# Kernel tuning notes

Hardware: AMD Instinct MI355X
Metric: run time of the kernel (lower is better)

Reference implementation:

```python
import jax, jax.numpy as jnp
import numpy as np
from jax import lax

B, C, H, W = 8, 512, 16, 16
Di, N, R, K = 1024, 16, 32, 4  # d_inner, d_state, dt_rank, num scan directions
EPS = 1e-5


def _ln(x, g, b):
    mu = x.mean(-1, keepdims=True)
    var = ((x - mu) ** 2).mean(-1, keepdims=True)
    return (x - mu) * lax.rsqrt(var + EPS) * g + b


def _ss2d_core(xc, x_proj_w, dt_w, dt_b, A_logs, Ds):
    # xc: (b, Di, H, W) after depthwise conv + SiLU. 4-direction selective scan.
    b = xc.shape[0]
    L = H * W
    x_flat = xc.reshape(b, Di, L)
    x_wh = xc.transpose(0, 1, 3, 2).reshape(b, Di, L)
    x_hwwh = jnp.stack([x_flat, x_wh], 1)                  # (b,2,Di,L)
    xs = jnp.concatenate([x_hwwh, x_hwwh[..., ::-1]], 1)   # (b,K,Di,L)
    x_dbl = jnp.einsum('bkdl,kcd->bkcl', xs, x_proj_w)     # (b,K,R+2N,L)
    dts, Bs, Cs = x_dbl[:, :, :R], x_dbl[:, :, R:R + N], x_dbl[:, :, R + N:]
    dts = jnp.einsum('bkrl,kdr->bkdl', dts, dt_w)
    delta = jax.nn.softplus(dts + dt_b[None, :, :, None])  # (b,K,Di,L)
    A = -jnp.exp(A_logs).reshape(K, Di, N)                 # (K,Di,N)

    def step(h, inp):
        d, u, Bl, Cl = inp  # d,u:(b,K,Di)  Bl,Cl:(b,K,N)
        h = jnp.exp(d[..., None] * A) * h + (d * u)[..., None] * Bl[:, :, None, :]
        yl = jnp.einsum('bkdn,bkn->bkd', h, Cl)
        return h, yl

    inps = (delta.transpose(3, 0, 1, 2), xs.transpose(3, 0, 1, 2),
            Bs.transpose(3, 0, 1, 2), Cs.transpose(3, 0, 1, 2))
    h0 = jnp.zeros((b, K, Di, N), xc.dtype)
    _, ys = lax.scan(step, h0, inps)                       # (L,b,K,Di)
    ys = ys.transpose(1, 2, 3, 0) + xs * Ds.reshape(1, K, Di, 1)  # + D*u skip
    inv = ys[:, 2:4, :, ::-1]
    wh = ys[:, 1].reshape(b, Di, W, H).transpose(0, 1, 3, 2).reshape(b, Di, L)
    invwh = inv[:, 1].reshape(b, Di, W, H).transpose(0, 1, 3, 2).reshape(b, Di, L)
    y = ys[:, 0] + inv[:, 0] + wh + invwh                  # (b,Di,L)
    return y.transpose(0, 2, 1).reshape(b, H, W, Di)


def _conv_ffn(x, ffn_conv_w, bn_g, bn_b, bn_mean, bn_var, fc1_w, fc2_w):
    x = lax.conv_general_dilated(x, ffn_conv_w, (1, 1), [(1, 1), (1, 1)],
                                 dimension_numbers=('NCHW', 'OIHW', 'NCHW'))
    x = ((x - bn_mean[:, None, None]) * lax.rsqrt(bn_var + EPS)[:, None, None]
         * bn_g[:, None, None] + bn_b[:, None, None])
    x = jnp.clip(x, 0.0, 6.0)                              # ReLU6
    x = jnp.einsum('bchw,oc->bohw', x, fc1_w)              # 1x1 conv fc1
    x = jax.nn.gelu(x, approximate=False)
    return jnp.einsum('bchw,oc->bohw', x, fc2_w)           # 1x1 conv fc2


def _forward(x, y, ln1_g, ln1_b, in_proj_w, conv_w, conv_b, x_proj_w, dt_w,
             dt_b, A_logs, Ds, out_norm_g, out_norm_b, out_proj_w, ffn_conv_w,
             bn_g, bn_b, bn_mean, bn_var, fc1_w, fc2_w, lin1_w, lin1_b,
             lin2_w, lin2_b):
    # --- VSSBlock: LN -> SS2D -> residual ---
    x1 = x.transpose(0, 2, 3, 1)                           # (B,H,W,C)
    xn = _ln(x1, ln1_g, ln1_b)
    xz = jnp.einsum('bhwc,oc->bhwo', xn, in_proj_w)        # in_proj (no bias)
    xa, z = xz[..., :Di], xz[..., Di:]
    xc = xa.transpose(0, 3, 1, 2)                          # (B,Di,H,W)
    xc = lax.conv_general_dilated(xc, conv_w, (1, 1), [(1, 1), (1, 1)],
                                  feature_group_count=Di,
                                  dimension_numbers=('NCHW', 'OIHW', 'NCHW'))
    xc = jax.nn.silu(xc + conv_b[:, None, None])
    yc = _ss2d_core(xc, x_proj_w, dt_w, dt_b, A_logs, Ds)  # (B,H,W,Di)
    yc = _ln(yc, out_norm_g, out_norm_b) * jax.nn.silu(z)
    vss = x1 + jnp.einsum('bhwd,od->bhwo', yc, out_proj_w)
    # --- ConvFFN ---
    xm = _conv_ffn(vss.transpose(0, 3, 1, 2), ffn_conv_w, bn_g, bn_b, bn_mean,
                   bn_var, fc1_w, fc2_w)                   # (B,C,H,W)
    # --- channel attention: both pools are AdaptiveAvgPool2d(1), so max==avg ---
    pooled = y.mean(axis=(2, 3))                           # (B,C)
    lin = jax.nn.relu(pooled @ lin1_w.T + lin1_b) @ lin2_w.T + lin2_b
    gate = jax.nn.sigmoid(2.0 * lin)                       # linear_max + linear_avg
    return gate[:, :, None, None] * xm


def setup_inputs() -> dict:
    key = jax.random.key(0)
    ks = jax.random.split(key, 16)
    n = lambda i, shape, s=0.05: jax.random.normal(ks[i], shape, jnp.float32) * s
    return {
        'x': n(0, (B, C, H, W), 1.0),
        'y': n(1, (B, C, H, W), 1.0),
        'ln1_g': jnp.ones((C,), jnp.float32), 'ln1_b': jnp.zeros((C,), jnp.float32),
        'in_proj_w': n(2, (2 * Di, C)),
        'conv_w': n(3, (Di, 1, 3, 3), 0.2), 'conv_b': jnp.zeros((Di,), jnp.float32),
        'x_proj_w': n(4, (K, R + 2 * N, Di)),
        'dt_w': n(5, (K, Di, R), 0.1), 'dt_b': n(6, (K, Di), 0.1),
        'A_logs': n(7, (K * Di, N), 0.1), 'Ds': jnp.ones((K * Di,), jnp.float32),
        'out_norm_g': jnp.ones((Di,), jnp.float32), 'out_norm_b': jnp.zeros((Di,), jnp.float32),
        'out_proj_w': n(8, (C, Di)),
        'ffn_conv_w': n(9, (C, C, 3, 3)),
        'bn_g': jnp.ones((C,), jnp.float32), 'bn_b': jnp.zeros((C,), jnp.float32),
        'bn_mean': jnp.zeros((C,), jnp.float32), 'bn_var': jnp.ones((C,), jnp.float32),
        'fc1_w': n(10, (C, C)), 'fc2_w': n(11, (C, C)),
        'lin1_w': n(12, (C // 2, C)), 'lin1_b': jnp.zeros((C // 2,), jnp.float32),
        'lin2_w': n(13, (C, C // 2)), 'lin2_b': jnp.zeros((C,), jnp.float32),
    }


def reference(x, y, ln1_g, ln1_b, in_proj_w, conv_w, conv_b, x_proj_w, dt_w,
              dt_b, A_logs, Ds, out_norm_g, out_norm_b, out_proj_w, ffn_conv_w,
              bn_g, bn_b, bn_mean, bn_var, fc1_w, fc2_w, lin1_w, lin1_b,
              lin2_w, lin2_b):
    return _forward(x, y, ln1_g, ln1_b, in_proj_w, conv_w, conv_b, x_proj_w,
                    dt_w, dt_b, A_logs, Ds, out_norm_g, out_norm_b, out_proj_w,
                    ffn_conv_w, bn_g, bn_b, bn_mean, bn_var, fc1_w, fc2_w,
                    lin1_w, lin1_b, lin2_w, lin2_b)
```

## Files before the change

kernel.cpp:

```cpp
#include <hip/hip_runtime.h>
#include <hip/hip_bf16.h>
#include <math.h>

#define DEV_INLINE __device__ __forceinline__

constexpr int B_ = 8, C_ = 512, L_ = 256;
constexpr float EPS_ = 1e-5f;

typedef __attribute__((ext_vector_type(8))) short bf16x8;
typedef __attribute__((ext_vector_type(4))) float f32x4;

DEV_INLINE int lmap1(int l) { return ((l & 15) << 4) | (l >> 4); }
DEV_INLINE float sigmoidf_(float x) { return 1.f / (1.f + __expf(-x)); }
DEV_INLINE float siluf_(float x) { return x * sigmoidf_(x); }

DEV_INLINE unsigned pk2(float a, float b) {
    __hip_bfloat16 x = __float2bfloat16(a), y = __float2bfloat16(b);
    unsigned short ux = *reinterpret_cast<unsigned short*>(&x);
    unsigned short uy = *reinterpret_cast<unsigned short*>(&y);
    return ((unsigned)uy << 16) | ux;
}

__global__ __launch_bounds__(256) void k_pool(const float* __restrict__ y, float* __restrict__ pooled) {
    int bc = blockIdx.x;
    int t = threadIdx.x;
    __shared__ float red[256];
    red[t] = y[bc * 256 + t];
    __syncthreads();
    for (int s = 128; s > 0; s >>= 1) { if (t < s) red[t] += red[t + s]; __syncthreads(); }
    if (t == 0) pooled[bc] = red[0] * (1.f / 256.f);
}

__global__ __launch_bounds__(256) void k_gate(const float* __restrict__ pooled,
                                              const float* __restrict__ lin1_w, const float* __restrict__ lin1_b,
                                              const float* __restrict__ lin2_w, const float* __restrict__ lin2_b,
                                              float* __restrict__ gate) {
    int b = blockIdx.x;
    int t = threadIdx.x;
    __shared__ float p[512];
    __shared__ float h1[256];
    p[t] = pooled[b * 512 + t];
    p[t + 256] = pooled[b * 512 + t + 256];
    __syncthreads();
    float s = lin1_b[t];
    for (int c = 0; c < 512; ++c) s = fmaf(p[c], lin1_w[t * 512 + c], s);
    h1[t] = fmaxf(s, 0.f);
    __syncthreads();
    #pragma unroll
    for (int cc = 0; cc < 2; ++cc) {
        int c = t + cc * 256;
        float s2 = lin2_b[c];
        for (int j = 0; j < 256; ++j) s2 = fmaf(h1[j], lin2_w[c * 256 + j], s2);
        gate[b * 512 + c] = sigmoidf_(2.f * s2);
    }
}

__global__ __launch_bounds__(256) void k_ln(const float* __restrict__ x, const float* __restrict__ g,
                                            const float* __restrict__ bta, float* __restrict__ xn) {
    int pos = blockIdx.x;
    int b = pos >> 8, l = pos & 255;
    int t = threadIdx.x;
    float v0 = x[(b * C_ + t) * L_ + l];
    float v1 = x[(b * C_ + t + 256) * L_ + l];
    __shared__ float red[256];
    red[t] = v0 + v1;
    __syncthreads();
    for (int s = 128; s > 0; s >>= 1) { if (t < s) red[t] += red[t + s]; __syncthreads(); }
    float mu = red[0] * (1.f / 512.f);
    __syncthreads();
    float d0 = v0 - mu, d1 = v1 - mu;
    red[t] = d0 * d0 + d1 * d1;
    __syncthreads();
    for (int s = 128; s > 0; s >>= 1) { if (t < s) red[t] += red[t + s]; __syncthreads(); }
    float rs = rsqrtf(red[0] * (1.f / 512.f) + EPS_);
    xn[pos * C_ + t] = d0 * rs * g[t] + bta[t];
    xn[pos * C_ + t + 256] = d1 * rs * g[t + 256] + bta[t + 256];
}

__global__ __launch_bounds__(256) void k_wcast5(const float* __restrict__ ip, const float* __restrict__ xp,
                                                const float* __restrict__ op, const float* __restrict__ f1,
                                                const float* __restrict__ f2, const float* __restrict__ dtw,
                                                __hip_bfloat16* __restrict__ dst) {
    size_t e = ((size_t)blockIdx.x * 256 + threadIdx.x) * 4;
    const float* src; size_t off;
    if (e < 1048576) { src = ip; off = e; }
    else if (e < 1310720) { src = xp; off = e - 1048576; }
    else if (e < 1835008) { src = op; off = e - 1310720; }
    else if (e < 2097152) { src = f1; off = e - 1835008; }
    else if (e < 2359296) { src = f2; off = e - 2097152; }
    else { src = dtw; off = e - 2359296; }
    float4 v = *(const float4*)(src + off);
    uint2 o; o.x = pk2(v.x, v.y); o.y = pk2(v.z, v.w);
    *(uint2*)(dst + e) = o;
}

enum { M_INPROJ = 0, M_XDBL = 1, M_OUTPROJ = 2, M_FC1 = 3, M_FC2 = 4, M_DELTA = 5 };

template <int MODE>
__global__ __launch_bounds__(256) void gemm_mfma(const float* __restrict__ Af, const __hip_bfloat16* __restrict__ Wb,
                                                 float* __restrict__ O, float* __restrict__ O2,
                                                 const float* __restrict__ AUX, __hip_bfloat16* __restrict__ Ob) {
    constexpr int KK = (MODE == M_XDBL || MODE == M_OUTPROJ) ? 1024 : (MODE == M_DELTA) ? 32 : 512;
    __shared__ short Asm[64 * 32];
    __shared__ short Bsm[64 * 32];
    const int t = threadIdx.x;
    const int lane = t & 63, wv = t >> 6;
    int m0, n0 = 0, kdir = 0, bq = 0;
    if constexpr (MODE == M_XDBL) { m0 = blockIdx.x * 64; kdir = blockIdx.y; }
    else if constexpr (MODE == M_FC2) { bq = blockIdx.x >> 3; m0 = (blockIdx.x & 7) * 64; n0 = blockIdx.y * 64; }
    else { m0 = blockIdx.x * 64; n0 = blockIdx.y * 64; }
    const int kdel = (m0 >> 8) & 3;

    const int r_ = t >> 2, kq = t & 3;
    const int skey = (r_ >> 1) & 3;
    uint4* adst = (uint4*)(Asm + r_ * 32) + (kq ^ skey);
    uint4* bdst = (uint4*)(Bsm + r_ * 32) + (kq ^ skey);

    const float* arowf = nullptr;
    const __hip_bfloat16* arowb = nullptr;
    if constexpr (MODE == M_INPROJ) arowf = Af + (size_t)(m0 + r_) * 512 + kq * 8;
    else if constexpr (MODE == M_XDBL) {
        int m = m0 + r_; int b = m >> 8, l = m & 255;
        int lm = (kdir < 2) ? l : 255 - l;
        arowf = Af + (size_t)((b * 2 + (kdir & 1)) * 256 + lm) * 1024 + kq * 8;
    } else if constexpr (MODE == M_OUTPROJ) arowf = Af + (size_t)(m0 + r_) * 1024 + kq * 8;
    else if constexpr (MODE == M_FC1) arowf = Af + (size_t)(m0 + r_) * 512 + kq * 8;
    else if constexpr (MODE == M_DELTA) arowf = Af + (size_t)(m0 + r_) * 64 + kq * 8;
    else arowb = Wb + (size_t)(m0 + r_) * 512 + kq * 8;

    const __hip_bfloat16* browb = nullptr;
    const float* browf = nullptr;
    if constexpr (MODE == M_INPROJ) browb = Wb + (size_t)(n0 + r_) * 512 + kq * 8;
    else if constexpr (MODE == M_XDBL) browb = Wb + (size_t)(kdir * 64 + r_) * 1024 + kq * 8;
    else if constexpr (MODE == M_OUTPROJ) browb = Wb + (size_t)(n0 + r_) * 1024 + kq * 8;
    else if constexpr (MODE == M_FC1) browb = Wb + (size_t)(n0 + r_) * 512 + kq * 8;
    else if constexpr (MODE == M_DELTA) browb = Wb + ((size_t)(kdel * 1024 + n0 + r_)) * 32 + kq * 8;
    else browf = Af + (size_t)(bq * 256 + n0 + r_) * 512 + kq * 8;

    f32x4 acc[4];
    #pragma unroll
    for (int nf = 0; nf < 4; ++nf) acc[nf] = (f32x4){0.f, 0.f, 0.f, 0.f};

    for (int k0 = 0; k0 < KK; k0 += 32) {
        __syncthreads();
        if constexpr (MODE == M_FC2) {
            *adst = *(const uint4*)(arowb + k0);
            float4 u0 = *(const float4*)(browf + k0);
            float4 u1 = *(const float4*)(browf + k0 + 4);
            uint4 pk; pk.x = pk2(u0.x, u0.y); pk.y = pk2(u0.z, u0.w); pk.z = pk2(u1.x, u1.y); pk.w = pk2(u1.z, u1.w);
            *bdst = pk;
        } else {
            float4 u0 = *(const float4*)(arowf + k0);
            float4 u1 = *(const float4*)(arowf + k0 + 4);
            uint4 pk; pk.x = pk2(u0.x, u0.y); pk.y = pk2(u0.z, u0.w); pk.z = pk2(u1.x, u1.y); pk.w = pk2(u1.z, u1.w);
            *adst = pk;
            *bdst = *(const uint4*)(browb + k0);
        }
        __syncthreads();
        int mrow = wv * 16 + (lane & 15);
        int ks = lane >> 4;
        bf16x8 af = *(const bf16x8*)(Asm + mrow * 32 + ((ks ^ ((mrow >> 1) & 3)) * 8));
        #pragma unroll
        for (int nf = 0; nf < 4; ++nf) {
            int nrow = nf * 16 + (lane & 15);
            bf16x8 bfv = *(const bf16x8*)(Bsm + nrow * 32 + ((ks ^ ((nrow >> 1) & 3)) * 8));
            acc[nf] = __builtin_amdgcn_mfma_f32_16x16x32_bf16(af, bfv, acc[nf], 0, 0, 0);
        }
    }

    const int mlb = (lane >> 4) * 4, nl = lane & 15;
    #pragma unroll
    for (int nf = 0; nf < 4; ++nf) {
        #pragma unroll
        for (int j = 0; j < 4; ++j) {
            float v = acc[nf][j];
            int m_loc = wv * 16 + mlb + j;
            int n_loc = nf * 16 + nl;
            if constexpr (MODE == M_INPROJ) {
                int m = m0 + m_loc, n = n0 + n_loc;
                if (n0 < 1024) O[(size_t)m * 1024 + n] = v;
                else O2[(size_t)m * 1024 + (n - 1024)] = v;
            } else if constexpr (MODE == M_XDBL) {
                int m = m0 + m_loc; int b = m >> 8, l = m & 255;
                O[((size_t)(b * 4 + kdir) * 256 + l) * 64 + n_loc] = v;
            } else if constexpr (MODE == M_OUTPROJ) {
                int m = m0 + m_loc, n = n0 + n_loc; int b = m >> 8, l = m & 255;
                float f = AUX[((size_t)b * 512 + n) * 256 + l] + v;
                Ob[(size_t)m * 512 + n] = __float2bfloat16(f);
            } else if constexpr (MODE == M_FC1) {
                int m = m0 + m_loc, n = n0 + n_loc;
                O[(size_t)m * 512 + n] = 0.5f * v * (1.f + erff(v * 0.70710678118f));
            } else if constexpr (MODE == M_DELTA) {
                int m = m0 + m_loc, n = n0 + n_loc;
                float v2 = v + AUX[kdel * 1024 + n];
                float dlt = (v2 > 20.f) ? v2 : __logf(1.f + __expf(v2));
                O[(size_t)m * 1024 + n] = dlt;
            } else {
                int c = m0 + m_loc, n = n0 + n_loc;
                O[((size_t)(bq * 512 + c)) * 256 + n] = v * AUX[bq * 512 + c];
            }
        }
    }
}

__global__ __launch_bounds__(256) void k_dwconv2(const float* __restrict__ xa, const float* __restrict__ cw,
                                                 const float* __restrict__ cb, float* __restrict__ xs_t) {
    int pos = blockIdx.x;
    int b = pos >> 8, l = pos & 255;
    int h = l >> 4, w = l & 15;
    int t = threadIdx.x;
    int d = t * 4;
    float wv[36];
    {
        const float4* cp = (const float4*)(cw + (size_t)d * 9);
        #pragma unroll
        for (int j = 0; j < 9; ++j) { float4 v = cp[j]; wv[j*4] = v.x; wv[j*4+1] = v.y; wv[j*4+2] = v.z; wv[j*4+3] = v.w; }
    }
    float4 bias = *(const float4*)(cb + d);
    float a0 = bias.x, a1 = bias.y, a2 = bias.z, a3 = bias.w;
    #pragma unroll
    for (int ky = -1; ky <= 1; ++ky) {
        int hh = h + ky;
        if ((unsigned)hh >= 16u) continue;
        #pragma unroll
        for (int kx = -1; kx <= 1; ++kx) {
            int ww = w + kx;
            if ((unsigned)ww >= 16u) continue;
            float4 v = *(const float4*)(xa + (size_t)(b * 256 + hh * 16 + ww) * 1024 + d);
            int tap = (ky + 1) * 3 + (kx + 1);
            a0 = fmaf(v.x, wv[0 * 9 + tap], a0);
            a1 = fmaf(v.y, wv[1 * 9 + tap], a1);
            a2 = fmaf(v.z, wv[2 * 9 + tap], a2);
            a3 = fmaf(v.w, wv[3 * 9 + tap], a3);
        }
    }
    float4 o; o.x = siluf_(a0); o.y = siluf_(a1); o.z = siluf_(a2); o.w = siluf_(a3);
    *(float4*)(xs_t + ((size_t)(b * 2 + 0) * 256 + l) * 1024 + d) = o;
    *(float4*)(xs_t + ((size_t)(b * 2 + 1) * 256 + lmap1(l)) * 1024 + d) = o;
}

__global__ __launch_bounds__(512) void k_scan5(const float* __restrict__ xs_t, const float* __restrict__ x_dbl,
                                               const float* __restrict__ A_logs, const float* __restrict__ Ds,
                                               float* __restrict__ ys_t) {
    const int bk = blockIdx.x >> 5;
    const int d0 = (blockIdx.x & 31) * 32;
    const int b = bk >> 2, k = bk & 3;
    const int t = threadIdx.x;
    const int c = t >> 5, dd = t & 31;
    const int d = d0 + dd;
    const bool rev = (k >= 2);

    __shared__ float Ssh[16][33];
    __shared__ float locH[16][32][17];

    float An2[16];
    {
        const float* alp = A_logs + (size_t)(k * 1024 + d) * 16;
        #pragma unroll
        for (int i = 0; i < 16; ++i) An2[i] = -__expf(alp[i]) * 1.44269504088896f;
    }
    const float Dv = Ds[k * 1024 + d];

    const float* up0 = xs_t + ((size_t)(b * 2 + (k & 1)) * 256 + (rev ? 255 : 0)) * 1024 + d;
    const ptrdiff_t ustr = rev ? -1024 : 1024;
    const float* xp = x_dbl + (size_t)bk * 256 * 64;
    float* yp = ys_t + (size_t)bk * 256 * 1024 + d;

    const int lbeg = c * 16;
    float h[16];
    #pragma unroll
    for (int i = 0; i < 16; ++i) h[i] = 0.f;
    float S = 0.f;

    #pragma unroll 4
    for (int l = lbeg; l < lbeg + 16; ++l) {
        float dl = yp[(size_t)l * 1024];
        float u = up0[(ptrdiff_t)l * ustr];
        S += dl;
        float du = dl * u;
        #pragma unroll
        for (int q = 0; q < 4; ++q) {
            float4 Bq = *(const float4*)(xp + l * 64 + 32 + q * 4);
            h[q*4+0] = fmaf(exp2f(dl * An2[q*4+0]), h[q*4+0], du * Bq.x);
            h[q*4+1] = fmaf(exp2f(dl * An2[q*4+1]), h[q*4+1], du * Bq.y);
            h[q*4+2] = fmaf(exp2f(dl * An2[q*4+2]), h[q*4+2], du * Bq.z);
            h[q*4+3] = fmaf(exp2f(dl * An2[q*4+3]), h[q*4+3], du * Bq.w);
        }
    }
    Ssh[c][dd] = S;
    #pragma unroll
    for (int i = 0; i < 16; ++i) locH[c][dd][i] = h[i];
    __syncthreads();

    #pragma unroll
    for (int i = 0; i < 16; ++i) h[i] = 0.f;
    for (int j = 0; j < c; ++j) {
        float Sj = Ssh[j][dd];
        #pragma unroll
        for (int i = 0; i < 16; ++i) h[i] = fmaf(exp2f(Sj * An2[i]), h[i], locH[j][dd][i]);
    }

    #pragma unroll 4
    for (int l = lbeg; l < lbeg + 16; ++l) {
        float dl = yp[(size_t)l * 1024];
        float u = up0[(ptrdiff_t)l * ustr];
        float du = dl * u;
        float yv = 0.f;
        #pragma unroll
        for (int q = 0; q < 4; ++q) {
            float4 Bq = *(const float4*)(xp + l * 64 + 32 + q * 4);
            float4 Cq = *(const float4*)(xp + l * 64 + 48 + q * 4);
            h[q*4+0] = fmaf(exp2f(dl * An2[q*4+0]), h[q*4+0], du * Bq.x); yv = fmaf(h[q*4+0], Cq.x, yv);
            h[q*4+1] = fmaf(exp2f(dl * An2[q*4+1]), h[q*4+1], du * Bq.y); yv = fmaf(h[q*4+1], Cq.y, yv);
            h[q*4+2] = fmaf(exp2f(dl * An2[q*4+2]), h[q*4+2], du * Bq.z); yv = fmaf(h[q*4+2], Cq.z, yv);
            h[q*4+3] = fmaf(exp2f(dl * An2[q*4+3]), h[q*4+3], du * Bq.w); yv = fmaf(h[q*4+3], Cq.w, yv);
        }
        yp[(size_t)l * 1024] = yv + u * Dv;
    }
}

__global__ __launch_bounds__(256) void k_combine(const float* __restrict__ ys_t, const float* __restrict__ z,
                                                 const float* __restrict__ g, const float* __restrict__ bb,
                                                 float* __restrict__ yc) {
    int pos = blockIdx.x;
    int b = pos >> 8, l = pos & 255;
    int t = threadIdx.x;
    int lw = lmap1(l);
    const float* r0 = ys_t + (size_t)((b * 4 + 0) * 256 + l) * 1024;
    const float* r1 = ys_t + (size_t)((b * 4 + 1) * 256 + lw) * 1024;
    const float* r2 = ys_t + (size_t)((b * 4 + 2) * 256 + (255 - l)) * 1024;
    const float* r3 = ys_t + (size_t)((b * 4 + 3) * 256 + (255 - lw)) * 1024;
    float v[4];
    float psum = 0.f;
    #pragma unroll
    for (int q = 0; q < 4; ++q) {
        int d = t + q * 256;
        v[q] = r0[d] + r1[d] + r2[d] + r3[d];
        psum += v[q];
    }
    __shared__ float red[256];
    red[t] = psum;
    __syncthreads();
    for (int s = 128; s > 0; s >>= 1) { if (t < s) red[t] += red[t + s]; __syncthreads(); }
    float mu = red[0] * (1.f / 1024.f);
    __syncthreads();
    float p2 = 0.f;
    #pragma unroll
    for (int q = 0; q < 4; ++q) { float dd = v[q] - mu; p2 += dd * dd; }
    red[t] = p2;
    __syncthreads();
    for (int s = 128; s > 0; s >>= 1) { if (t < s) red[t] += red[t + s]; __syncthreads(); }
    float rs = rsqrtf(red[0] * (1.f / 1024.f) + EPS_);
    #pragma unroll
    for (int q = 0; q < 4; ++q) {
        int d = t + q * 256;
        float zn = z[(size_t)pos * 1024 + d];
        yc[(size_t)pos * 1024 + d] = ((v[q] - mu) * rs * g[d] + bb[d]) * siluf_(zn);
    }
}

__global__ __launch_bounds__(256) void k_wcast(const float* __restrict__ w, __hip_bfloat16* __restrict__ wt) {
    int gid = blockIdx.x * 256 + threadIdx.x;
    const float* src = w + (size_t)gid * 9;
    #pragma unroll
    for (int tap = 0; tap < 9; ++tap) wt[(size_t)tap * 262144 + gid] = __float2bfloat16(src[tap]);
}

__global__ __launch_bounds__(256) void k_conv2m(const __hip_bfloat16* __restrict__ vssb,
                                                const __hip_bfloat16* __restrict__ wt,
                                                float* __restrict__ convp) {
    __shared__ short Asm[18 * 18 * 32];
    __shared__ short Bsm[9 * 64 * 32];
    const int b = blockIdx.x, co0 = blockIdx.y * 64, split = blockIdx.z;
    const int t = threadIdx.x;
    const int lane = t & 63, wid = t >> 6;
    const int wcol = lane & 15, slot = lane >> 4;

    f32x4 acc[4][4];
    #pragma unroll
    for (int r = 0; r < 4; ++r)
        #pragma unroll
        for (int g = 0; g < 4; ++g) acc[r][g] = (f32x4){0.f, 0.f, 0.f, 0.f};

    for (int ch = 0; ch < 4; ++ch) {
        const int ci0 = split * 128 + ch * 32;
        __syncthreads();
        for (int i = t; i < 324; i += 256) {
            int row = i / 18, col = i - row * 18;
            uint4 v0 = {0,0,0,0}, v1 = {0,0,0,0}, v2 = {0,0,0,0}, v3 = {0,0,0,0};
            if (row >= 1 && row <= 16 && col >= 1 && col <= 16) {
                const uint4* src = (const uint4*)(vssb + ((size_t)(b * 256 + (row - 1) * 16 + (col - 1)) * 512 + ci0));
                v0 = src[0]; v1 = src[1]; v2 = src[2]; v3 = src[3];
            }
            uint4* dst = (uint4*)(Asm + i * 32);
            int key = (col >> 1) & 3;
            dst[0 ^ key] = v0; dst[1 ^ key] = v1; dst[2 ^ key] = v2; dst[3 ^ key] = v3;
        }
        for (int i = t; i < 576; i += 256) {
            int tap = i >> 6, col = i & 63;
            const uint4* src = (const uint4*)(wt + ((size_t)(tap * 512 + co0 + col) * 512 + ci0));
            uint4* dst = (uint4*)(Bsm + i * 32);
            int key = (col >> 1) & 3;
            dst[0 ^ key] = src[0]; dst[1 ^ key] = src[1]; dst[2 ^ key] = src[2]; dst[3 ^ key] = src[3];
        }
        __syncthreads();
        #pragma unroll
        for (int tap = 0; tap < 9; ++tap) {
            const int ky = tap / 3, kx = tap - ky * 3;
            bf16x8 af[4], bfr[4];
            #pragma unroll
            for (int r = 0; r < 4; ++r) {
                int crow = wid * 4 + r + ky;
                int ccol = wcol + kx;
                int s2 = slot ^ ((ccol >> 1) & 3);
                af[r] = *(const bf16x8*)(Asm + ((crow * 18 + ccol) * 32 + s2 * 8));
            }
            #pragma unroll
            for (int g = 0; g < 4; ++g) {
                int col = g * 16 + wcol;
                int s2 = slot ^ ((col >> 1) & 3);
                bfr[g] = *(const bf16x8*)(Bsm + ((tap * 64 + col) * 32 + s2 * 8));
            }
            #pragma unroll
            for (int r = 0; r < 4; ++r)
                #pragma unroll
                for (int g = 0; g < 4; ++g)
                    acc[r][g] = __builtin_amdgcn_mfma_f32_16x16x32_bf16(af[r], bfr[g], acc[r][g], 0, 0, 0);
        }
    }
    float* base = convp + (size_t)split * 1048576 + (size_t)b * 512 * 256;
    #pragma unroll
    for (int r = 0; r < 4; ++r) {
        int h = wid * 4 + r;
        #pragma unroll
        for (int g = 0; g < 4; ++g) {
            int co = co0 + g * 16 + wcol;
            *(f32x4*)(base + (size_t)co * 256 + h * 16 + slot * 4) = acc[r][g];
        }
    }
}

__global__ __launch_bounds__(256) void k_convred2(const float* __restrict__ convp,
                                                  const float* __restrict__ bn_g, const float* __restrict__ bn_b,
                                                  const float* __restrict__ bn_mean, const float* __restrict__ bn_var,
                                                  float* __restrict__ t1) {
    int b = blockIdx.x >> 7, cb = (blockIdx.x >> 3) & 15, pb = blockIdx.x & 7;
    int co0 = cb * 32, pos0 = pb * 32;
    int t = threadIdx.x;
    int ti = t >> 5, tj = t & 31;
    __shared__ float tile[32][33];
    #pragma unroll
    for (int r = 0; r < 4; ++r) {
        int co = co0 + ti + r * 8;
        size_t idx = ((size_t)b * 512 + co) * 256 + pos0 + tj;
        float s = convp[idx] + convp[idx + 1048576] + convp[idx + 2097152] + convp[idx + 3145728];
        float o = (s - bn_mean[co]) * rsqrtf(bn_var[co] + EPS_) * bn_g[co] + bn_b[co];
        tile[ti + r * 8][tj] = fminf(fmaxf(o, 0.f), 6.f);
    }
    __syncthreads();
    #pragma unroll
    for (int r = 0; r < 4; ++r) {
        int pos = pos0 + ti + r * 8;
        t1[((size_t)b * 256 + pos) * 512 + co0 + tj] = tile[tj][ti + r * 8];
    }
}

extern "C" void kernel_launch(void* const* d_in, const int* in_sizes, int n_in,
                              void* d_out, int out_size, void* d_ws, size_t ws_size,
                              hipStream_t stream) {
    const float* x = (const float*)d_in[0];
    const float* y = (const float*)d_in[1];
    const float* ln1_g = (const float*)d_in[2];
    const float* ln1_b = (const float*)d_in[3];
    const float* in_proj_w = (const float*)d_in[4];
    const float* conv_w = (const float*)d_in[5];
    const float* conv_b = (const float*)d_in[6];
    const float* x_proj_w = (const float*)d_in[7];
    const float* dt_w = (const float*)d_in[8];
    const float* dt_b = (const float*)d_in[9];
    const float* A_logs = (const float*)d_in[10];
    const float* Ds = (const float*)d_in[11];
    const float* out_norm_g = (const float*)d_in[12];
    const float* out_norm_b = (const float*)d_in[13];
    const float* out_proj_w = (const float*)d_in[14];
    const float* ffn_conv_w = (const float*)d_in[15];
    const float* bn_g = (const float*)d_in[16];
    const float* bn_b = (const float*)d_in[17];
    const float* bn_mean = (const float*)d_in[18];
    const float* bn_var = (const float*)d_in[19];
    const float* fc1_w = (const float*)d_in[20];
    const float* fc2_w = (const float*)d_in[21];
    const float* lin1_w = (const float*)d_in[22];
    const float* lin1_b = (const float*)d_in[23];
    const float* lin2_w = (const float*)d_in[24];
    const float* lin2_b = (const float*)d_in[25];
    float* out = (float*)d_out;

    char* ws = (char*)d_ws;
    size_t off = 0;
    auto alloc = [&](size_t nf) { float* p = (float*)(ws + off); off += nf * sizeof(float); return p; };
    float* xn    = alloc(2048u * 512);
    float* xa    = alloc(2048u * 1024);
    float* z     = alloc(2048u * 1024);
    float* xs_t  = alloc(2u * 2048 * 1024);
    float* x_dbl = alloc(8u * 4 * 256 * 64);
    float* ys_t  = alloc(4u * 2048 * 1024);
    float* wb    = alloc(1245184);
    float* pooled = alloc(4096);
    float* gate   = alloc(4096);

    float* yc = xa;
    float* t1 = xs_t;
    float* t2 = xs_t + 2048u * 512;
    __hip_bfloat16* vssb = (__hip_bfloat16*)xn;
    __hip_bfloat16* w_t  = (__hip_bfloat16*)z;
    float* convp = ys_t;
    __hip_bfloat16* inprojb = (__hip_bfloat16*)wb;
    __hip_bfloat16* xprojb  = inprojb + 1048576;
    __hip_bfloat16* outprojb = xprojb + 262144;
    __hip_bfloat16* fc1b = outprojb + 524288;
    __hip_bfloat16* fc2b = fc1b + 262144;
    __hip_bfloat16* dtwb = fc2b + 262144;

    k_wcast5<<<2432, 256, 0, stream>>>(in_proj_w, x_proj_w, out_proj_w, fc1_w, fc2_w, dt_w, inprojb);
    k_pool<<<4096, 256, 0, stream>>>(y, pooled);
    k_gate<<<8, 256, 0, stream>>>(pooled, lin1_w, lin1_b, lin2_w, lin2_b, gate);
    k_ln<<<2048, 256, 0, stream>>>(x, ln1_g, ln1_b, xn);
    gemm_mfma<M_INPROJ><<<dim3(32, 32), 256, 0, stream>>>(xn, inprojb, xa, z, nullptr, nullptr);
    k_dwconv2<<<2048, 256, 0, stream>>>(xa, conv_w, conv_b, xs_t);
    gemm_mfma<M_XDBL><<<dim3(32, 4), 256, 0, stream>>>(xs_t, xprojb, x_dbl, nullptr, nullptr, nullptr);
    gemm_mfma<M_DELTA><<<dim3(128, 16), 256, 0, stream>>>(x_dbl, dtwb, ys_t, nullptr, dt_b, nullptr);
    k_scan5<<<1024, 512, 0, stream>>>(xs_t, x_dbl, A_logs, Ds, ys_t);
    k_combine<<<2048, 256, 0, stream>>>(ys_t, z, out_norm_g, out_norm_b, yc);
    k_wcast<<<1024, 256, 0, stream>>>(ffn_conv_w, w_t);
    gemm_mfma<M_OUTPROJ><<<dim3(32, 8), 256, 0, stream>>>(yc, outprojb, nullptr, nullptr, x, vssb);
    k_conv2m<<<dim3(8, 8, 4), 256, 0, stream>>>(vssb, w_t, convp);
    k_convred2<<<1024, 256, 0, stream>>>(convp, bn_g, bn_b, bn_mean, bn_var, t1);
    gemm_mfma<M_FC1><<<dim3(32, 8), 256, 0, stream>>>(t1, fc1b, t2, nullptr, nullptr, nullptr);
    gemm_mfma<M_FC2><<<dim3(64, 4), 256, 0, stream>>>(t2, fc2b, out, nullptr, gate, nullptr);
}
```

Before: 293.0 us.

## Tile delta/ys buffer by 32-channel blocks so scan accesses stay contiguous

The delta buffer written by the dt GEMM, and overwritten in place by the scan outputs, moves from a (bk, l, d) layout to a blocked (bk, d/32, l, 32) layout. Each scan block's 32 channels over 256 steps then sit in one contiguous 32 KB chunk, where the old layout read 128-byte pieces strided by 4 KB. The GEMM epilogue and the combine kernel are rewritten to the same layout. The cost is scattered 128-byte-segment reads in combine and a less regular store pattern in the GEMM epilogue.

```diff
diff --git a/kernel.cpp b/kernel.cpp
--- a/kernel.cpp
+++ b/kernel.cpp
@@ -192,9 +192,10 @@
                 O[(size_t)m * 512 + n] = 0.5f * v * (1.f + erff(v * 0.70710678118f));
             } else if constexpr (MODE == M_DELTA) {
                 int m = m0 + m_loc, n = n0 + n_loc;
+                int bkk = m >> 8, l = m & 255;
                 float v2 = v + AUX[kdel * 1024 + n];
                 float dlt = (v2 > 20.f) ? v2 : __logf(1.f + __expf(v2));
-                O[(size_t)m * 1024 + n] = dlt;
+                O[((((size_t)bkk * 32) + (n >> 5)) * 256 + l) * 32 + (n & 31)] = dlt;
             } else {
                 int c = m0 + m_loc, n = n0 + n_loc;
                 O[((size_t)(bq * 512 + c)) * 256 + n] = v * AUX[bq * 512 + c];
@@ -239,15 +240,15 @@
     *(float4*)(xs_t + ((size_t)(b * 2 + 1) * 256 + lmap1(l)) * 1024 + d) = o;
 }
 
-__global__ __launch_bounds__(512) void k_scan5(const float* __restrict__ xs_t, const float* __restrict__ x_dbl,
+__global__ __launch_bounds__(512) void k_scan6(const float* __restrict__ xs_t, const float* __restrict__ x_dbl,
                                                const float* __restrict__ A_logs, const float* __restrict__ Ds,
-                                               float* __restrict__ ys_t) {
+                                               float* __restrict__ dys) {
     const int bk = blockIdx.x >> 5;
-    const int d0 = (blockIdx.x & 31) * 32;
+    const int db = blockIdx.x & 31;
     const int b = bk >> 2, k = bk & 3;
     const int t = threadIdx.x;
     const int c = t >> 5, dd = t & 31;
-    const int d = d0 + dd;
+    const int d = db * 32 + dd;
     const bool rev = (k >= 2);
 
     __shared__ float Ssh[16][33];
@@ -261,26 +262,26 @@
     }
     const float Dv = Ds[k * 1024 + d];
 
-    const float* up0 = xs_t + ((size_t)(b * 2 + (k & 1)) * 256 + (rev ? 255 : 0)) * 1024 + d;
+    const int lbeg = c * 16;
+    float* yp = dys + (((size_t)bk * 32 + db) * 256 + lbeg) * 32 + dd;
+    const float* up = xs_t + ((size_t)(b * 2 + (k & 1)) * 256 + (rev ? 255 - lbeg : lbeg)) * 1024 + d;
     const ptrdiff_t ustr = rev ? -1024 : 1024;
-    const float* xp = x_dbl + (size_t)bk * 256 * 64;
-    float* yp = ys_t + (size_t)bk * 256 * 1024 + d;
-
-    const int lbeg = c * 16;
+    const float* xc = x_dbl + (size_t)bk * 256 * 64 + lbeg * 64;
+
     float h[16];
     #pragma unroll
     for (int i = 0; i < 16; ++i) h[i] = 0.f;
     float S = 0.f;
 
     #pragma unroll 4
-    for (int l = lbeg; l < lbeg + 16; ++l) {
-        float dl = yp[(size_t)l * 1024];
-        float u = up0[(ptrdiff_t)l * ustr];
+    for (int li = 0; li < 16; ++li) {
+        float dl = yp[li * 32];
+        float u = up[(ptrdiff_t)li * ustr];
         S += dl;
         float du = dl * u;
         #pragma unroll
         for (int q = 0; q < 4; ++q) {
-            float4 Bq = *(const float4*)(xp + l * 64 + 32 + q * 4);
+            float4 Bq = *(const float4*)(xc + li * 64 + 32 + q * 4);
             h[q*4+0] = fmaf(exp2f(dl * An2[q*4+0]), h[q*4+0], du * Bq.x);
             h[q*4+1] = fmaf(exp2f(dl * An2[q*4+1]), h[q*4+1], du * Bq.y);
             h[q*4+2] = fmaf(exp2f(dl * An2[q*4+2]), h[q*4+2], du * Bq.z);
@@ -301,41 +302,42 @@
     }
 
     #pragma unroll 4
-    for (int l = lbeg; l < lbeg + 16; ++l) {
-        float dl = yp[(size_t)l * 1024];
-        float u = up0[(ptrdiff_t)l * ustr];
+    for (int li = 0; li < 16; ++li) {
+        float dl = yp[li * 32];
+        float u = up[(ptrdiff_t)li * ustr];
         float du = dl * u;
         float yv = 0.f;
         #pragma unroll
         for (int q = 0; q < 4; ++q) {
-            float4 Bq = *(const float4*)(xp + l * 64 + 32 + q * 4);
-            float4 Cq = *(const float4*)(xp + l * 64 + 48 + q * 4);
+            float4 Bq = *(const float4*)(xc + li * 64 + 32 + q * 4);
+            float4 Cq = *(const float4*)(xc + li * 64 + 48 + q * 4);
             h[q*4+0] = fmaf(exp2f(dl * An2[q*4+0]), h[q*4+0], du * Bq.x); yv = fmaf(h[q*4+0], Cq.x, yv);
             h[q*4+1] = fmaf(exp2f(dl * An2[q*4+1]), h[q*4+1], du * Bq.y); yv = fmaf(h[q*4+1], Cq.y, yv);
             h[q*4+2] = fmaf(exp2f(dl * An2[q*4+2]), h[q*4+2], du * Bq.z); yv = fmaf(h[q*4+2], Cq.z, yv);
             h[q*4+3] = fmaf(exp2f(dl * An2[q*4+3]), h[q*4+3], du * Bq.w); yv = fmaf(h[q*4+3], Cq.w, yv);
         }
-        yp[(size_t)l * 1024] = yv + u * Dv;
-    }
-}
-
-__global__ __launch_bounds__(256) void k_combine(const float* __restrict__ ys_t, const float* __restrict__ z,
+        yp[li * 32] = yv + u * Dv;
+    }
+}
+
+__global__ __launch_bounds__(256) void k_combine(const float* __restrict__ dys, const float* __restrict__ z,
                                                  const float* __restrict__ g, const float* __restrict__ bb,
                                                  float* __restrict__ yc) {
     int pos = blockIdx.x;
     int b = pos >> 8, l = pos & 255;
     int t = threadIdx.x;
     int lw = lmap1(l);
-    const float* r0 = ys_t + (size_t)((b * 4 + 0) * 256 + l) * 1024;
-    const float* r1 = ys_t + (size_t)((b * 4 + 1) * 256 + lw) * 1024;
-    const float* r2 = ys_t + (size_t)((b * 4 + 2) * 256 + (255 - l)) * 1024;
-    const float* r3 = ys_t + (size_t)((b * 4 + 3) * 256 + (255 - lw)) * 1024;
+    int db0 = t >> 5, dd = t & 31;
     float v[4];
     float psum = 0.f;
     #pragma unroll
     for (int q = 0; q < 4; ++q) {
-        int d = t + q * 256;
-        v[q] = r0[d] + r1[d] + r2[d] + r3[d];
+        int dbq = db0 + q * 8;
+        float s0 = dys[((((size_t)(b * 4 + 0) * 32) + dbq) * 256 + l) * 32 + dd];
+        float s1 = dys[((((size_t)(b * 4 + 1) * 32) + dbq) * 256 + lw) * 32 + dd];
+        float s2 = dys[((((size_t)(b * 4 + 2) * 32) + dbq) * 256 + (255 - l)) * 32 + dd];
+        float s3 = dys[((((size_t)(b * 4 + 3) * 32) + dbq) * 256 + (255 - lw)) * 32 + dd];
+        v[q] = s0 + s1 + s2 + s3;
         psum += v[q];
     }
     __shared__ float red[256];
@@ -346,14 +348,14 @@
     __syncthreads();
     float p2 = 0.f;
     #pragma unroll
-    for (int q = 0; q < 4; ++q) { float dd = v[q] - mu; p2 += dd * dd; }
+    for (int q = 0; q < 4; ++q) { float ddv = v[q] - mu; p2 += ddv * ddv; }
     red[t] = p2;
     __syncthreads();
     for (int s = 128; s > 0; s >>= 1) { if (t < s) red[t] += red[t + s]; __syncthreads(); }
     float rs = rsqrtf(red[0] * (1.f / 1024.f) + EPS_);
     #pragma unroll
     for (int q = 0; q < 4; ++q) {
-        int d = t + q * 256;
+        int d = (db0 + q * 8) * 32 + dd;
         float zn = z[(size_t)pos * 1024 + d];
         yc[(size_t)pos * 1024 + d] = ((v[q] - mu) * rs * g[d] + bb[d]) * siluf_(zn);
     }
@@ -530,7 +532,7 @@
     k_dwconv2<<<2048, 256, 0, stream>>>(xa, conv_w, conv_b, xs_t);
     gemm_mfma<M_XDBL><<<dim3(32, 4), 256, 0, stream>>>(xs_t, xprojb, x_dbl, nullptr, nullptr, nullptr);
     gemm_mfma<M_DELTA><<<dim3(128, 16), 256, 0, stream>>>(x_dbl, dtwb, ys_t, nullptr, dt_b, nullptr);
-    k_scan5<<<1024, 512, 0, stream>>>(xs_t, x_dbl, A_logs, Ds, ys_t);
+    k_scan6<<<1024, 512, 0, stream>>>(xs_t, x_dbl, A_logs, Ds, ys_t);
     k_combine<<<2048, 256, 0, stream>>>(ys_t, z, out_norm_g, out_norm_b, yc);
     k_wcast<<<1024, 256, 0, stream>>>(ffn_conv_w, w_t);
     gemm_mfma<M_OUTPROJ><<<dim3(32, 8), 256, 0, stream>>>(yc, outprojb, nullptr, nullptr, x, vssb);
```

New measurement: 295.2 us. No clear change (+0.8%).
